# Optimization experiments

Measured on AMD Instinct MI355X. Metric: run time of the kernel, lower is better.

## Reference

```python
import jax, jax.numpy as jnp
import numpy as np

B, T, D = 8, 4096, 64

def setup_inputs() -> dict:
    key = jax.random.key(0)
    k1, k2 = jax.random.split(key)
    inputs = jax.random.normal(k1, (B, T, D), dtype=jnp.float32)
    # keras 'random_normal' initializer: stddev 0.05
    W = jax.random.normal(k2, (D, D), dtype=jnp.float32) * 0.05
    return {"inputs": inputs, "W": W}

def reference(inputs, W):
    # q = inputs @ W               : [B,T,D]
    # a = q @ inputs^T             : [B,T,T] (no scaling, bias b unused in original)
    # out = softmax(a, -1) @ inputs: [B,T,D]
    q = jnp.einsum('btd,de->bte', inputs, W)
    scores = jnp.einsum('btd,bsd->bts', q, inputs)
    attn = jax.nn.softmax(scores, axis=-1)
    return jnp.einsum('bts,bsd->btd', attn, inputs)
```

## Files before the change

kernel.cpp:

```cpp
#include <hip/hip_runtime.h>

typedef _Float16 f16;
typedef _Float16 f16x8 __attribute__((ext_vector_type(8)));
typedef __bf16 bf16x8 __attribute__((ext_vector_type(8)));
typedef __bf16 bf16x4 __attribute__((ext_vector_type(4)));
typedef float floatx4 __attribute__((ext_vector_type(4)));
typedef unsigned short u16;
typedef unsigned int u32;

#define B_N   8
#define T_SEQ 4096
#define DIM   64
#define QT    64
#define KT    128
#define NIT   (T_SEQ / KT)
#define PSTR  40
#define OSTR  68
#define XSTR  72
#define LOG2E 1.44269504f
#define FRAG  512
#define KTILE_FRAGS 16

#if __has_builtin(__builtin_amdgcn_exp2f)
#define EXP2(x) __builtin_amdgcn_exp2f(x)
#else
#define EXP2(x) exp2f(x)
#endif

__launch_bounds__(256, 2)
__global__ void prep_kernel(const float* __restrict__ X, const float* __restrict__ W,
                            u16* __restrict__ Kswz, u16* __restrict__ Qswz,
                            u16* __restrict__ Vswz) {
  __shared__ __attribute__((aligned(16))) u16 Xs[DIM * XSTR];
  __shared__ __attribute__((aligned(16))) u16 Wt[DIM * XSTR];
  __shared__ __attribute__((aligned(16))) u16 Qs[DIM * XSTR];
  const int tid = threadIdx.x;
  const int lane = tid & 63, w = tid >> 6, qd = lane >> 4, ln = lane & 15;
  const int b = blockIdx.y;
  const int t0 = blockIdx.x * 64;
  const long xbase = ((long)b * T_SEQ + t0) * DIM;

  {
    const int r = tid >> 2, c0 = (tid & 3) * 16;
    float v[16];
#pragma unroll
    for (int i = 0; i < 4; i++)
      *(float4*)&v[i * 4] = *(const float4*)(X + xbase + (long)r * DIM + c0 + i * 4);
    u16 h[16];
#pragma unroll
    for (int j = 0; j < 16; j++) h[j] = __builtin_bit_cast(u16, (f16)v[j]);
    *(uint4*)&Xs[r * XSTR + c0] = *(uint4*)&h[0];
    *(uint4*)&Xs[r * XSTR + c0 + 8] = *(uint4*)&h[8];
    float wv[16];
#pragma unroll
    for (int i = 0; i < 4; i++)
      *(float4*)&wv[i * 4] = *(const float4*)(W + r * DIM + c0 + i * 4);
#pragma unroll
    for (int j = 0; j < 16; j++) Wt[(c0 + j) * XSTR + r] = __builtin_bit_cast(u16, (f16)wv[j]);
  }
  __syncthreads();

  {
    const long R = (long)b * (T_SEQ / 16) + blockIdx.x * 4 + w;
#pragma unroll
    for (int ks = 0; ks < 2; ks++) {
      f16x8 kv = *(const f16x8*)&Xs[(w * 16 + ln) * XSTR + ks * 32 + qd * 8];
      *(f16x8*)(Kswz + (R * 2 + ks) * FRAG + lane * 8) = kv;
    }
  }

  {
    const int wq = w * 16;
    floatx4 acc[4];
#pragma unroll
    for (int ct = 0; ct < 4; ct++) acc[ct] = (floatx4)0.0f;
#pragma unroll
    for (int ks = 0; ks < 2; ks++) {
      f16x8 aX = *(const f16x8*)&Xs[(wq + ln) * XSTR + ks * 32 + qd * 8];
#pragma unroll
      for (int ct = 0; ct < 4; ct++) {
        f16x8 bW = *(const f16x8*)&Wt[(ct * 16 + ln) * XSTR + ks * 32 + qd * 8];
        acc[ct] = __builtin_amdgcn_mfma_f32_16x16x32_f16(aX, bW, acc[ct], 0, 0, 0);
      }
    }
#pragma unroll
    for (int ct = 0; ct < 4; ct++)
#pragma unroll
      for (int r = 0; r < 4; r++)
        Qs[(wq + qd * 4 + r) * XSTR + ct * 16 + ln] =
            __builtin_bit_cast(u16, (f16)(acc[ct][r] * LOG2E));
  }

  {
    const long Cb = (long)b * 4 + w;
    const int J0 = blockIdx.x * 2;
#pragma unroll
    for (int J = 0; J < 2; J++) {
      bf16x8 vv;
#pragma unroll
      for (int j = 0; j < 8; j++) {
        f16 hv = __builtin_bit_cast(f16, Xs[(J * 32 + qd * 8 + j) * XSTR + w * 16 + ln]);
        vv[j] = (__bf16)(float)hv;
      }
      *(bf16x8*)(Vswz + (Cb * (T_SEQ / 32) + J0 + J) * FRAG + lane * 8) = vv;
    }
  }

  {
    const long R = (long)b * (T_SEQ / 16) + blockIdx.x * 4 + w;
#pragma unroll
    for (int ks = 0; ks < 2; ks++) {
      f16x8 qv = *(const f16x8*)&Qs[(w * 16 + ln) * XSTR + ks * 32 + qd * 8];
      *(f16x8*)(Qswz + (R * 2 + ks) * FRAG + lane * 8) = qv;
    }
  }
}

__device__ __forceinline__ void attn_step(
    const u16* __restrict__ pKf, const u16* __restrict__ pVf, u16* __restrict__ Pw,
    f16x8 (&kbuf)[2][2], const f16x8 (&aQ)[4][2],
    floatx4 (&O)[4][4], float (&lacc)[4], int ktCur, int ln, int qd) {
  const long voff = (long)ktCur * (4 * FRAG);
  bf16x8 bV[4];
#pragma unroll
  for (int cd = 0; cd < 4; cd++)
    bV[cd] = *(const bf16x8*)(pVf + voff + (long)cd * ((T_SEQ / 32) * FRAG));

  floatx4 St[2][4];
#pragma unroll
  for (int ct = 0; ct < 2; ct++)
#pragma unroll
    for (int rb = 0; rb < 4; rb++) St[ct][rb] = (floatx4)0.0f;
#pragma unroll
  for (int ks = 0; ks < 2; ks++)
#pragma unroll
    for (int ct = 0; ct < 2; ct++)
#pragma unroll
      for (int rb = 0; rb < 4; rb++)
        St[ct][rb] = __builtin_amdgcn_mfma_f32_16x16x32_f16(kbuf[ct][ks], aQ[rb][ks], St[ct][rb], 0, 0, 0);

  const long koffn = (long)((ktCur + 2) & (NIT - 1)) * (KTILE_FRAGS * FRAG);
#pragma unroll
  for (int ct = 0; ct < 2; ct++)
#pragma unroll
    for (int ks = 0; ks < 2; ks++)
      kbuf[ct][ks] = *(const f16x8*)(pKf + koffn + (ct * 2 + ks) * FRAG);

#pragma unroll
  for (int rb = 0; rb < 4; rb++)
#pragma unroll
    for (int ct = 0; ct < 2; ct++) {
      bf16x4 pk;
      float ps = 0.f;
#pragma unroll
      for (int r = 0; r < 4; r++) {
        float p = EXP2(St[ct][rb][r]);
        ps += p;
        pk[r] = (__bf16)p;
      }
      lacc[rb] += ps;
      *(uint2*)&Pw[(rb * 16 + ln) * PSTR + ct * 16 + qd * 4] = __builtin_bit_cast(uint2, pk);
    }

#pragma unroll
  for (int rb = 0; rb < 4; rb++) {
    bf16x8 aP = *(const bf16x8*)&Pw[(rb * 16 + ln) * PSTR + qd * 8];
#pragma unroll
    for (int cd = 0; cd < 4; cd++)
      O[rb][cd] = __builtin_amdgcn_mfma_f32_16x16x32_bf16(aP, bV[cd], O[rb][cd], 0, 0, 0);
  }
}

__launch_bounds__(256, 2)
__global__ void attn_kernel(const u16* __restrict__ Kswz, const u16* __restrict__ Qswz,
                            const u16* __restrict__ Vswz, float* __restrict__ out) {
  __shared__ __attribute__((aligned(16))) u16 Ps[2][4 * QT * PSTR];
  __shared__ __attribute__((aligned(16))) float Opart[4 * 16 * OSTR];
  __shared__ float lpart[4][QT];

  const int tid = threadIdx.x;
  const int lane = tid & 63;
  const int w = tid >> 6;
  const int qd = lane >> 4;
  const int ln = lane & 15;
  const int bid = blockIdx.x;
  const int b = bid & 7;
  const int q0 = (bid >> 3) * QT;
  const long bbase = (long)b * T_SEQ * DIM;

  const u16* pKf = Kswz + ((long)b * (T_SEQ / 16) + w * 2) * 2 * FRAG + lane * 8;
  const u16* pVf = Vswz + ((long)b * 4) * (T_SEQ / 32) * FRAG + (long)w * FRAG + lane * 8;
  u16* Pw0 = &Ps[0][w * (QT * PSTR)];
  u16* Pw1 = &Ps[1][w * (QT * PSTR)];

  f16x8 aQ[4][2];
#pragma unroll
  for (int rb = 0; rb < 4; rb++)
#pragma unroll
    for (int ks = 0; ks < 2; ks++)
      aQ[rb][ks] = *(const f16x8*)(Qswz +
          (((long)b * (T_SEQ / 16) + (q0 >> 4) + rb) * 2 + ks) * FRAG + lane * 8);

  floatx4 O[4][4];
  float lacc[4] = {0.f, 0.f, 0.f, 0.f};
#pragma unroll
  for (int rb = 0; rb < 4; rb++)
#pragma unroll
    for (int cd = 0; cd < 4; cd++) O[rb][cd] = (floatx4)0.0f;

  f16x8 bKa[2][2], bKb[2][2];
#pragma unroll
  for (int ct = 0; ct < 2; ct++)
#pragma unroll
    for (int ks = 0; ks < 2; ks++) {
      bKa[ct][ks] = *(const f16x8*)(pKf + (ct * 2 + ks) * FRAG);
      bKb[ct][ks] = *(const f16x8*)(pKf + KTILE_FRAGS * FRAG + (ct * 2 + ks) * FRAG);
    }

#pragma unroll 1
  for (int kt = 0; kt < NIT; kt += 2) {
    attn_step(pKf, pVf, Pw0, bKa, aQ, O, lacc, kt, ln, qd);
    attn_step(pKf, pVf, Pw1, bKb, aQ, O, lacc, kt + 1, ln, qd);
  }

#pragma unroll
  for (int rb = 0; rb < 4; rb++) {
    float v = lacc[rb];
    v += __shfl_xor(v, 16, 64);
    v += __shfl_xor(v, 32, 64);
    if (qd == 0) lpart[w][rb * 16 + ln] = v;
  }

  const int erow = tid >> 4;
  const int ec0 = (tid & 15) * 4;
#pragma unroll 1
  for (int rb = 0; rb < 4; rb++) {
    __syncthreads();
#pragma unroll
    for (int cd = 0; cd < 4; cd++)
#pragma unroll
      for (int r = 0; r < 4; r++)
        Opart[w * 16 * OSTR + (qd * 4 + r) * OSTR + cd * 16 + ln] = O[rb][cd][r];
    __syncthreads();
    float4 s0 = *(const float4*)&Opart[0 * 16 * OSTR + erow * OSTR + ec0];
    float4 s1 = *(const float4*)&Opart[1 * 16 * OSTR + erow * OSTR + ec0];
    float4 s2 = *(const float4*)&Opart[2 * 16 * OSTR + erow * OSTR + ec0];
    float4 s3 = *(const float4*)&Opart[3 * 16 * OSTR + erow * OSTR + ec0];
    float l = lpart[0][rb * 16 + erow] + lpart[1][rb * 16 + erow] +
              lpart[2][rb * 16 + erow] + lpart[3][rb * 16 + erow];
    float inv = 1.0f / l;
    float4 o;
    o.x = (s0.x + s1.x + s2.x + s3.x) * inv;
    o.y = (s0.y + s1.y + s2.y + s3.y) * inv;
    o.z = (s0.z + s1.z + s2.z + s3.z) * inv;
    o.w = (s0.w + s1.w + s2.w + s3.w) * inv;
    *(float4*)(out + bbase + (long)(q0 + rb * 16 + erow) * DIM + ec0) = o;
  }
}

extern "C" void kernel_launch(void* const* d_in, const int* in_sizes, int n_in,
                              void* d_out, int out_size, void* d_ws, size_t ws_size,
                              hipStream_t stream) {
  const float* X = (const float*)d_in[0];
  const float* W = (const float*)d_in[1];
  float* out = (float*)d_out;
  const size_t SZ = (size_t)B_N * T_SEQ * DIM * 2;
  u16* Kswz = (u16*)d_ws;
  u16* Qswz = (u16*)((char*)d_ws + SZ);
  u16* Vswz = (u16*)((char*)d_ws + 2 * SZ);
  prep_kernel<<<dim3(T_SEQ / 64, B_N), 256, 0, stream>>>(X, W, Kswz, Qswz, Vswz);
  attn_kernel<<<dim3(B_N * (T_SEQ / QT)), 256, 0, stream>>>(Kswz, Qswz, Vswz, out);
}
```

Measured before the change: 113.7 us.

## Split key dimension across eight waves per block and alias Opart onto P buffer

Doubles the block size to 512 threads so that eight waves each handle a slice of a 256-key tile, halving the sequential key loop per wave. The P scratch buffer is now single-buffered per wave and reused as the partial-O reduction area, which reduces LDS per block. The epilogue reduces eight partial accumulators per row with float2 stores. This raises register and occupancy pressure under launch_bounds(512,4) and lengthens the cross-wave reduction.

```diff
diff --git a/kernel.cpp b/kernel.cpp
--- a/kernel.cpp
+++ b/kernel.cpp
@@ -12,14 +12,14 @@
 #define T_SEQ 4096
 #define DIM   64
 #define QT    64
-#define KT    128
+#define KT    256
 #define NIT   (T_SEQ / KT)
 #define PSTR  40
 #define OSTR  68
 #define XSTR  72
 #define LOG2E 1.44269504f
 #define FRAG  512
-#define KTILE_FRAGS 16
+#define KTILE_FRAGS 32
 
 #if __has_builtin(__builtin_amdgcn_exp2f)
 #define EXP2(x) __builtin_amdgcn_exp2f(x)
@@ -120,7 +120,7 @@
     const u16* __restrict__ pKf, const u16* __restrict__ pVf, u16* __restrict__ Pw,
     f16x8 (&kbuf)[2][2], const f16x8 (&aQ)[4][2],
     floatx4 (&O)[4][4], float (&lacc)[4], int ktCur, int ln, int qd) {
-  const long voff = (long)ktCur * (4 * FRAG);
+  const long voff = (long)ktCur * (8 * FRAG);
   bf16x8 bV[4];
 #pragma unroll
   for (int cd = 0; cd < 4; cd++)
@@ -171,12 +171,13 @@
   }
 }
 
-__launch_bounds__(256, 2)
+__launch_bounds__(512, 4)
 __global__ void attn_kernel(const u16* __restrict__ Kswz, const u16* __restrict__ Qswz,
                             const u16* __restrict__ Vswz, float* __restrict__ out) {
-  __shared__ __attribute__((aligned(16))) u16 Ps[2][4 * QT * PSTR];
-  __shared__ __attribute__((aligned(16))) float Opart[4 * 16 * OSTR];
-  __shared__ float lpart[4][QT];
+  __shared__ __attribute__((aligned(16))) u16 Ps[8 * QT * PSTR];
+  __shared__ float lpart[8][QT];
+
+  float* Opart = (float*)Ps;
 
   const int tid = threadIdx.x;
   const int lane = tid & 63;
@@ -190,8 +191,7 @@
 
   const u16* pKf = Kswz + ((long)b * (T_SEQ / 16) + w * 2) * 2 * FRAG + lane * 8;
   const u16* pVf = Vswz + ((long)b * 4) * (T_SEQ / 32) * FRAG + (long)w * FRAG + lane * 8;
-  u16* Pw0 = &Ps[0][w * (QT * PSTR)];
-  u16* Pw1 = &Ps[1][w * (QT * PSTR)];
+  u16* Pw = &Ps[w * (QT * PSTR)];
 
   f16x8 aQ[4][2];
 #pragma unroll
@@ -219,8 +219,8 @@
 
 #pragma unroll 1
   for (int kt = 0; kt < NIT; kt += 2) {
-    attn_step(pKf, pVf, Pw0, bKa, aQ, O, lacc, kt, ln, qd);
-    attn_step(pKf, pVf, Pw1, bKb, aQ, O, lacc, kt + 1, ln, qd);
+    attn_step(pKf, pVf, Pw, bKa, aQ, O, lacc, kt, ln, qd);
+    attn_step(pKf, pVf, Pw, bKb, aQ, O, lacc, kt + 1, ln, qd);
   }
 
 #pragma unroll
@@ -231,8 +231,8 @@
     if (qd == 0) lpart[w][rb * 16 + ln] = v;
   }
 
-  const int erow = tid >> 4;
-  const int ec0 = (tid & 15) * 4;
+  const int erow = tid >> 5;
+  const int ec = (tid & 31) * 2;
 #pragma unroll 1
   for (int rb = 0; rb < 4; rb++) {
     __syncthreads();
@@ -242,19 +242,16 @@
       for (int r = 0; r < 4; r++)
         Opart[w * 16 * OSTR + (qd * 4 + r) * OSTR + cd * 16 + ln] = O[rb][cd][r];
     __syncthreads();
-    float4 s0 = *(const float4*)&Opart[0 * 16 * OSTR + erow * OSTR + ec0];
-    float4 s1 = *(const float4*)&Opart[1 * 16 * OSTR + erow * OSTR + ec0];
-    float4 s2 = *(const float4*)&Opart[2 * 16 * OSTR + erow * OSTR + ec0];
-    float4 s3 = *(const float4*)&Opart[3 * 16 * OSTR + erow * OSTR + ec0];
-    float l = lpart[0][rb * 16 + erow] + lpart[1][rb * 16 + erow] +
-              lpart[2][rb * 16 + erow] + lpart[3][rb * 16 + erow];
+    float sx = 0.f, sy = 0.f, l = 0.f;
+#pragma unroll
+    for (int ww = 0; ww < 8; ww++) {
+      float2 s = *(const float2*)&Opart[ww * 16 * OSTR + erow * OSTR + ec];
+      sx += s.x; sy += s.y;
+      l += lpart[ww][rb * 16 + erow];
+    }
     float inv = 1.0f / l;
-    float4 o;
-    o.x = (s0.x + s1.x + s2.x + s3.x) * inv;
-    o.y = (s0.y + s1.y + s2.y + s3.y) * inv;
-    o.z = (s0.z + s1.z + s2.z + s3.z) * inv;
-    o.w = (s0.w + s1.w + s2.w + s3.w) * inv;
-    *(float4*)(out + bbase + (long)(q0 + rb * 16 + erow) * DIM + ec0) = o;
+    float2 o; o.x = sx * inv; o.y = sy * inv;
+    *(float2*)(out + bbase + (long)(q0 + rb * 16 + erow) * DIM + ec) = o;
   }
 }
 
@@ -269,5 +266,5 @@
   u16* Qswz = (u16*)((char*)d_ws + SZ);
   u16* Vswz = (u16*)((char*)d_ws + 2 * SZ);
   prep_kernel<<<dim3(T_SEQ / 64, B_N), 256, 0, stream>>>(X, W, Kswz, Qswz, Vswz);
-  attn_kernel<<<dim3(B_N * (T_SEQ / QT)), 256, 0, stream>>>(Kswz, Qswz, Vswz, out);
-}
+  attn_kernel<<<dim3(B_N * (T_SEQ / QT)), 512, 0, stream>>>(Kswz, Qswz, Vswz, out);
+}
```

New measurement: 424.9 us. 274% more time.
